# Kernel tuning notes

Measured on AMD Instinct MI355X. Metric: run time of the kernel, lower is better.

Reference implementation:

```python
import jax, jax.numpy as jnp
import numpy as np

B, S, H = 2, 2048, 2048
NH, NKV, HD = 16, 4, 128
GROUPS = NH // NKV  # 4
ROPE_BASE = 10000.0


def _rope_tables(seq_len, dim):
    inv_freq = 1.0 / (ROPE_BASE ** (jnp.arange(0, dim, 2, dtype=jnp.float32) / dim))
    t = jnp.arange(seq_len, dtype=jnp.float32)
    freqs = jnp.outer(t, inv_freq)            # [S, HD/2]
    emb = jnp.concatenate([freqs, freqs], -1)  # [S, HD]
    return jnp.cos(emb), jnp.sin(emb)


def _rotate_half(x):
    x1, x2 = x[..., : x.shape[-1] // 2], x[..., x.shape[-1] // 2:]
    return jnp.concatenate([-x2, x1], axis=-1)


def setup_inputs() -> dict:
    key = jax.random.key(0)
    ks = jax.random.split(key, 5)
    hidden_states = jax.random.normal(ks[0], (B, S, H), dtype=jnp.float32)
    wq = jax.random.normal(ks[1], (H, NH * HD), dtype=jnp.float32) * 0.02
    wk = jax.random.normal(ks[2], (H, NKV * HD), dtype=jnp.float32) * 0.02
    wv = jax.random.normal(ks[3], (H, NKV * HD), dtype=jnp.float32) * 0.02
    wo = jax.random.normal(ks[4], (NH * HD, H), dtype=jnp.float32) * 0.02
    # additive causal mask [1,1,S,S]
    causal = jnp.tril(jnp.ones((S, S), dtype=bool))
    attention_mask = jnp.where(causal, 0.0, jnp.finfo(jnp.float32).min)[None, None]
    return {"hidden_states": hidden_states, "attention_mask": attention_mask,
            "wq": wq, "wk": wk, "wv": wv, "wo": wo}


def reference(hidden_states, attention_mask, wq, wk, wv, wo):
    b, s, _ = hidden_states.shape
    # projections -> [B, heads, S, HD]
    q = (hidden_states @ wq).reshape(b, s, NH, HD).transpose(0, 2, 1, 3)
    k = (hidden_states @ wk).reshape(b, s, NKV, HD).transpose(0, 2, 1, 3)
    v = (hidden_states @ wv).reshape(b, s, NKV, HD).transpose(0, 2, 1, 3)
    cos, sin = _rope_tables(s, HD)             # [S, HD]
    cos = cos[None, None]; sin = sin[None, None]
    q = q * cos + _rotate_half(q) * sin
    k = k * cos + _rotate_half(k) * sin
    # GQA: repeat kv heads (matches repeat_interleave on dim=1)
    k = jnp.repeat(k, GROUPS, axis=1)
    v = jnp.repeat(v, GROUPS, axis=1)
    scores = jnp.einsum("bhqd,bhkd->bhqk", q, k) / jnp.sqrt(jnp.float32(HD))
    scores = scores + attention_mask
    probs = jax.nn.softmax(scores.astype(jnp.float32), axis=-1).astype(q.dtype)
    attn = jnp.einsum("bhqk,bhkd->bhqd", probs, v)
    attn = attn.transpose(0, 2, 1, 3).reshape(b, s, NH * HD)
    return attn @ wo
```

## Files before the change

### kernel.cpp

```cpp
#include <hip/hip_runtime.h>

typedef unsigned short u16;
typedef unsigned int u32;
typedef __attribute__((ext_vector_type(8))) __bf16 bf16x8;
typedef __attribute__((ext_vector_type(8))) u16 u16x8;
typedef __attribute__((ext_vector_type(4))) float f32x4;

#define B_ 2
#define S_ 2048
#define H_ 2048
#define NH_ 16
#define NKV_ 4
#define HD_ 128

__device__ __forceinline__ u16 f2bf(float f) {
  return __builtin_bit_cast(u16, static_cast<__bf16>(f));
}
__device__ __forceinline__ float bf2f(u16 v) {
  return __builtin_bit_cast(float, (u32)v << 16);
}
__device__ __forceinline__ void gl2lds16(const void* g, void* l) {
  __builtin_amdgcn_global_load_lds((const __attribute__((address_space(1))) u32*)g,
                                   (__attribute__((address_space(3))) u32*)l, 16, 0, 0);
}
__device__ __forceinline__ f32x4 mfma16(bf16x8 a, bf16x8 b, f32x4 c) {
  return __builtin_amdgcn_mfma_f32_16x16x32_bf16(a, b, c, 0, 0, 0);
}

__global__ __launch_bounds__(256) void cvt_f32_bf16(const float* __restrict__ in,
                                                    u16* __restrict__ out) {
  size_t i = ((size_t)blockIdx.x * 256 + threadIdx.x) * 8;
  const float4* p = (const float4*)(in + i);
  float4 a = p[0], b = p[1];
  u16x8 o;
  o[0] = f2bf(a.x); o[1] = f2bf(a.y); o[2] = f2bf(a.z); o[3] = f2bf(a.w);
  o[4] = f2bf(b.x); o[5] = f2bf(b.y); o[6] = f2bf(b.z); o[7] = f2bf(b.w);
  *(u16x8*)(out + i) = o;
}

__global__ __launch_bounds__(256) void transpose_qkv(const float* __restrict__ wq,
                                                     const float* __restrict__ wk,
                                                     const float* __restrict__ wv,
                                                     u16* __restrict__ out) {
  __shared__ float tl[32][33];
  int bx = blockIdx.x, by = blockIdx.y;
  int tx = threadIdx.x & 31, ty = threadIdx.x >> 5;
  int orow0 = bx * 32;
  const float* src;
  int scol0, C;
  if (orow0 < 2048)      { src = wq; scol0 = orow0;        C = 2048; }
  else if (orow0 < 2560) { src = wk; scol0 = orow0 - 2048; C = 512; }
  else                   { src = wv; scol0 = orow0 - 2560; C = 512; }
#pragma unroll
  for (int i = 0; i < 32; i += 8)
    tl[ty + i][tx] = src[(size_t)(by * 32 + ty + i) * C + scol0 + tx];
  __syncthreads();
#pragma unroll
  for (int i = 0; i < 32; i += 8)
    out[(size_t)(orow0 + ty + i) * 2048 + by * 32 + tx] = f2bf(tl[tx][ty + i]);
}

__global__ __launch_bounds__(256) void transpose_f32_bf16(const float* __restrict__ in,
                                                          u16* __restrict__ out,
                                                          int R, int C) {
  __shared__ float tl[32][33];
  int bx = blockIdx.x, by = blockIdx.y;
  int tx = threadIdx.x & 31, ty = threadIdx.x >> 5;
#pragma unroll
  for (int i = 0; i < 32; i += 8)
    tl[ty + i][tx] = in[(size_t)(by * 32 + ty + i) * C + bx * 32 + tx];
  __syncthreads();
#pragma unroll
  for (int i = 0; i < 32; i += 8)
    out[(size_t)(bx * 32 + ty + i) * R + by * 32 + tx] = f2bf(tl[tx][ty + i]);
}

__global__ __launch_bounds__(256) void transpose_v(const u16* __restrict__ kvb,
                                                   u16* __restrict__ vt) {
  __shared__ u16 tl[32][33];
  int sx = blockIdx.x, dx = blockIdx.y, b = blockIdx.z;
  int tx = threadIdx.x & 31, ty = threadIdx.x >> 5;
#pragma unroll
  for (int i = 0; i < 32; i += 8)
    tl[ty + i][tx] = kvb[(size_t)(b * S_ + sx * 32 + ty + i) * 1024 + 512 + dx * 32 + tx];
  __syncthreads();
#pragma unroll
  for (int i = 0; i < 32; i += 8)
    vt[(size_t)(b * 512 + dx * 32 + ty + i) * 2048 + sx * 32 + tx] = tl[tx][ty + i];
}

__global__ __launch_bounds__(256) void rope_kernel(u16* __restrict__ buf, int rstride,
                                                   int nhshift, float scale) {
  int idx = blockIdx.x * 256 + threadIdx.x;
  int grp = idx & 7;
  int h = (idx >> 3) & ((1 << nhshift) - 1);
  int tok = idx >> (3 + nhshift);
  int s = tok & (S_ - 1);
  u16* p = buf + (size_t)tok * rstride + (h << 7) + grp * 8;
  u16x8 lo = *(u16x8*)p;
  u16x8 hi = *(u16x8*)(p + 64);
  u16x8 olo, ohi;
#pragma unroll
  for (int j = 0; j < 8; j++) {
    int i = grp * 8 + j;
    float inv = exp2f((float)i * -0.20762050593045702f);
    float ang = (float)s * inv;
    float c = cosf(ang) * scale, sn = sinf(ang) * scale;
    float xl = bf2f(lo[j]), xh = bf2f(hi[j]);
    olo[j] = f2bf(xl * c - xh * sn);
    ohi[j] = f2bf(xh * c + xl * sn);
  }
  *(u16x8*)p = olo;
  *(u16x8*)(p + 64) = ohi;
}

template <int MODE>
__global__ __launch_bounds__(256) void gemm_bt(const u16* __restrict__ A,
                                               const u16* __restrict__ BT,
                                               void* __restrict__ C0,
                                               void* __restrict__ C1,
                                               int M, int N, int K) {
  __shared__ u16 As[2 * 128 * 32];
  __shared__ u16 Bs[2 * 128 * 32];
  const int Mt = M >> 7;
  const int nwg = gridDim.x;
  int wg = (blockIdx.x & 7) * (nwg >> 3) + (blockIdx.x >> 3);
  int tm = wg % Mt, tn = wg / Mt;
  const size_t m0 = (size_t)tm << 7, n0 = (size_t)tn << 7;
  const int tid = threadIdx.x;
  const int w = tid >> 6, lane = tid & 63;
  const int g = lane >> 4, l15 = lane & 15;
  const int wr = w >> 1, wc = w & 1;

  const int r0 = tid >> 2, s0 = tid & 3;
  const int r1 = (tid + 256) >> 2, s1 = (tid + 256) & 3;
  const u16* Ar0 = A + (m0 + r0) * K + s0 * 8;
  const u16* Ar1 = A + (m0 + r1) * K + s1 * 8;
  const u16* Br0 = BT + (n0 + r0) * K + s0 * 8;
  const u16* Br1 = BT + (n0 + r1) * K + s1 * 8;

  const f32x4 Z4 = {0.f, 0.f, 0.f, 0.f};
  f32x4 acc[4][4];
#pragma unroll
  for (int m = 0; m < 4; m++)
#pragma unroll
    for (int n = 0; n < 4; n++) acc[m][n] = Z4;

  gl2lds16(Ar0, &As[w * 512]);
  gl2lds16(Ar1, &As[w * 512 + 2048]);
  gl2lds16(Br0, &Bs[w * 512]);
  gl2lds16(Br1, &Bs[w * 512 + 2048]);

  const int nk = K >> 5;
  int cur = 0;
  for (int t = 0; t < nk; ++t) {
    if (t + 1 < nk) {
      const int k0 = (t + 1) << 5;
      const int nb = (cur ^ 1) << 12;
      gl2lds16(Ar0 + k0, &As[nb + w * 512]);
      gl2lds16(Ar1 + k0, &As[nb + w * 512 + 2048]);
      gl2lds16(Br0 + k0, &Bs[nb + w * 512]);
      gl2lds16(Br1 + k0, &Bs[nb + w * 512 + 2048]);
      asm volatile("s_waitcnt vmcnt(4)" ::: "memory");
    } else {
      asm volatile("s_waitcnt vmcnt(0)" ::: "memory");
    }
    __builtin_amdgcn_sched_barrier(0);
    __builtin_amdgcn_s_barrier();
    __builtin_amdgcn_sched_barrier(0);
    const int cb = cur << 12;
    bf16x8 af[4], bfr[4];
#pragma unroll
    for (int m = 0; m < 4; m++)
      af[m] = *(const bf16x8*)&As[cb + (wr * 64 + m * 16 + l15) * 32 + g * 8];
#pragma unroll
    for (int n = 0; n < 4; n++)
      bfr[n] = *(const bf16x8*)&Bs[cb + (wc * 64 + n * 16 + l15) * 32 + g * 8];
#pragma unroll
    for (int m = 0; m < 4; m++)
#pragma unroll
      for (int n = 0; n < 4; n++) acc[m][n] = mfma16(af[m], bfr[n], acc[m][n]);
    __builtin_amdgcn_sched_barrier(0);
    __builtin_amdgcn_s_barrier();
    __builtin_amdgcn_sched_barrier(0);
    cur ^= 1;
  }

  if (MODE == 2) {
    float* C = (float*)C0;
#pragma unroll
    for (int m = 0; m < 4; m++)
#pragma unroll
      for (int n = 0; n < 4; n++)
#pragma unroll
        for (int r = 0; r < 4; r++) {
          size_t row = m0 + wr * 64 + m * 16 + g * 4 + r;
          size_t col = n0 + wc * 64 + n * 16 + l15;
          C[row * (size_t)N + col] = acc[m][n][r];
        }
  } else {
    u16* C;
    size_t cs, cbase;
    if (n0 < 2048) { C = (u16*)C0; cs = 2048; cbase = n0; }
    else           { C = (u16*)C1; cs = 1024; cbase = n0 - 2048; }
#pragma unroll
    for (int m = 0; m < 4; m++)
#pragma unroll
      for (int n = 0; n < 4; n++)
#pragma unroll
        for (int r = 0; r < 4; r++) {
          size_t row = m0 + wr * 64 + m * 16 + g * 4 + r;
          C[row * cs + cbase + wc * 64 + n * 16 + l15] = f2bf(acc[m][n][r]);
        }
  }
}

__global__ __launch_bounds__(256) void attn_kernel(const u16* __restrict__ Qb,
                                                   const u16* __restrict__ KVb,
                                                   const u16* __restrict__ Vt,
                                                   u16* __restrict__ Ob) {
  __shared__ u16 Ks[2][64 * 128];
  __shared__ u16 Vs[2][128 * 64];
  __shared__ u16 Ps[4][16 * 72];
  const int pair = blockIdx.x, h = blockIdx.y, b = blockIdx.z;
  const int kvh = h >> 2;
  const int tid = threadIdx.x, w = tid >> 6, lane = tid & 63;
  const int g = lane >> 4, l15 = lane & 15;
  const f32x4 Z4 = {0.f, 0.f, 0.f, 0.f};
  u16x8 oneu;
#pragma unroll
  for (int j = 0; j < 8; j++) oneu[j] = 0x3f80;
  const bf16x8 ones = __builtin_bit_cast(bf16x8, oneu);

  const u16* Kbase = KVb + (size_t)b * S_ * 1024 + kvh * 128;
  const u16* Vbase = Vt + (size_t)(b * NKV_ + kvh) * HD_ * 2048;

  for (int half = 0; half < 2; ++half) {
    const int qt = half ? pair : 31 - pair;
    const int qrow0 = qt * 64 + w * 16;

    bf16x8 qf[4];
    const u16* qp = Qb + (size_t)(b * S_ + qrow0 + l15) * 2048 + h * 128;
#pragma unroll
    for (int ds = 0; ds < 4; ds++) qf[ds] = *(const bf16x8*)(qp + ds * 32 + g * 8);

    float m_r[4], l_r[4];
    f32x4 oa[8];
#pragma unroll
    for (int r = 0; r < 4; r++) { m_r[r] = -1e30f; l_r[r] = 0.f; }
#pragma unroll
    for (int n = 0; n < 8; n++) oa[n] = Z4;

    const int nt = qt + 1;
#pragma unroll
    for (int ro = 0; ro < 4; ++ro) {
      int c = ro * 256 + tid;
      int kv = c >> 4, p = c & 15;
      gl2lds16(Kbase + (size_t)kv * 1024 + 8 * (p ^ (kv & 15)), &Ks[0][ro * 2048 + w * 512]);
      int d = c >> 3, p2 = c & 7;
      gl2lds16(Vbase + (size_t)d * 2048 + 8 * (p2 ^ (d & 7)), &Vs[0][ro * 2048 + w * 512]);
    }
    __syncthreads();
    int cur = 0;

    for (int t = 0; t < nt; ++t) {
      const int kv0 = t * 64;
      if (t + 1 < nt) {
        const int nkv0 = kv0 + 64;
#pragma unroll
        for (int ro = 0; ro < 4; ++ro) {
          int c = ro * 256 + tid;
          int kv = c >> 4, p = c & 15;
          gl2lds16(Kbase + (size_t)(nkv0 + kv) * 1024 + 8 * (p ^ (kv & 15)),
                   &Ks[cur ^ 1][ro * 2048 + w * 512]);
          int d = c >> 3, p2 = c & 7;
          gl2lds16(Vbase + (size_t)d * 2048 + nkv0 + 8 * (p2 ^ (d & 7)),
                   &Vs[cur ^ 1][ro * 2048 + w * 512]);
        }
      }

      f32x4 sa[4];
#pragma unroll
      for (int c16 = 0; c16 < 4; c16++) sa[c16] = Z4;
      __builtin_amdgcn_s_setprio(1);
#pragma unroll
      for (int ds = 0; ds < 4; ++ds) {
#pragma unroll
        for (int c16 = 0; c16 < 4; ++c16) {
          bf16x8 kf = *(const bf16x8*)&Ks[cur][(c16 * 16 + l15) * 128 + ((ds * 4 + g) ^ l15) * 8];
          sa[c16] = mfma16(qf[ds], kf, sa[c16]);
        }
      }
      __builtin_amdgcn_s_setprio(0);

      if (kv0 + 63 > qrow0) {
#pragma unroll
        for (int c16 = 0; c16 < 4; c16++)
#pragma unroll
          for (int r = 0; r < 4; r++) {
            if (kv0 + c16 * 16 + l15 > qrow0 + g * 4 + r) sa[c16][r] = -1e30f;
          }
      }

      float lmax[4];
#pragma unroll
      for (int r = 0; r < 4; r++)
        lmax[r] = fmaxf(fmaxf(sa[0][r], sa[1][r]), fmaxf(sa[2][r], sa[3][r]));
      bool need = (lmax[0] > m_r[0] + 11.5415603f) || (lmax[1] > m_r[1] + 11.5415603f) ||
                  (lmax[2] > m_r[2] + 11.5415603f) || (lmax[3] > m_r[3] + 11.5415603f);
      if (__any(need)) {
        float pm[4];
#pragma unroll
        for (int r = 0; r < 4; r++) pm[r] = lmax[r];
#pragma unroll
        for (int off = 1; off < 16; off <<= 1)
#pragma unroll
          for (int r = 0; r < 4; r++) pm[r] = fmaxf(pm[r], __shfl_xor(pm[r], off));
#pragma unroll
        for (int r = 0; r < 4; r++) {
          float mn = fmaxf(m_r[r], pm[r]);
          float corr = exp2f(m_r[r] - mn);
          m_r[r] = mn;
          l_r[r] *= corr;
#pragma unroll
          for (int n = 0; n < 8; n++) oa[n][r] *= corr;
        }
      }

#pragma unroll
      for (int c16 = 0; c16 < 4; c16++)
#pragma unroll
        for (int r = 0; r < 4; r++)
          Ps[w][(g * 4 + r) * 72 + c16 * 16 + l15] =
              f2bf(exp2f(sa[c16][r] - m_r[r]));
      asm volatile("s_waitcnt lgkmcnt(0)" ::: "memory");
      __builtin_amdgcn_sched_barrier(0);

      f32x4 srow = Z4;
      __builtin_amdgcn_s_setprio(1);
#pragma unroll
      for (int ks = 0; ks < 2; ++ks) {
        bf16x8 pa = *(const bf16x8*)&Ps[w][l15 * 72 + ks * 32 + g * 8];
        srow = mfma16(pa, ones, srow);
#pragma unroll
        for (int n = 0; n < 8; n++) {
          bf16x8 vf = *(const bf16x8*)&Vs[cur][(n * 16 + l15) * 64 + (((ks * 4 + g) ^ (l15 & 7))) * 8];
          oa[n] = mfma16(pa, vf, oa[n]);
        }
      }
      __builtin_amdgcn_s_setprio(0);
#pragma unroll
      for (int r = 0; r < 4; r++) l_r[r] += srow[r];

      __syncthreads();
      cur ^= 1;
    }

    float inv[4];
#pragma unroll
    for (int r = 0; r < 4; r++) inv[r] = 1.0f / l_r[r];
#pragma unroll
    for (int n = 0; n < 8; n++)
#pragma unroll
      for (int r = 0; r < 4; r++) {
        size_t row = (size_t)b * S_ + qrow0 + g * 4 + r;
        Ob[row * 2048 + h * 128 + n * 16 + l15] = f2bf(oa[n][r] * inv[r]);
      }
  }
}

extern "C" void kernel_launch(void* const* d_in, const int* in_sizes, int n_in,
                              void* d_out, int out_size, void* d_ws, size_t ws_size,
                              hipStream_t stream) {
  const float* hid = (const float*)d_in[0];
  const float* wq = (const float*)d_in[2];
  const float* wk = (const float*)d_in[3];
  const float* wv = (const float*)d_in[4];
  const float* wo = (const float*)d_in[5];
  float* out = (float*)d_out;
  char* ws = (char*)d_ws;

  u16* hb     = (u16*)(ws);
  u16* wqkvT  = (u16*)(ws + (16u << 20));
  u16* Vt     = (u16*)(ws + (16u << 20));
  u16* woT    = (u16*)(ws + (20u << 20));
  u16* Qb     = (u16*)(ws + (28u << 20));
  u16* KVb    = (u16*)(ws + (44u << 20));

  cvt_f32_bf16<<<4096, 256, 0, stream>>>(hid, hb);
  transpose_qkv<<<dim3(96, 64), 256, 0, stream>>>(wq, wk, wv, wqkvT);

  gemm_bt<1><<<768, 256, 0, stream>>>(hb, wqkvT, Qb, KVb, 4096, 3072, 2048);

  rope_kernel<<<2048, 256, 0, stream>>>(Qb, 2048, 4, 0.1275179064f);
  rope_kernel<<<512, 256, 0, stream>>>(KVb, 1024, 2, 1.0f);

  transpose_v<<<dim3(64, 16, 2), 256, 0, stream>>>(KVb, Vt);
  transpose_f32_bf16<<<dim3(64, 64), 256, 0, stream>>>(wo, woT, 2048, 2048);

  attn_kernel<<<dim3(16, 16, 2), 256, 0, stream>>>(Qb, KVb, Vt, hb);

  gemm_bt<2><<<512, 256, 0, stream>>>(hb, woT, out, nullptr, 4096, 2048, 2048);
}
```

Before: 233.6 us.

## Fuse hidden-state bf16 conversion into QKV GEMM and tabulate RoPE cos/sin

```diff
diff --git a/kernel.cpp b/kernel.cpp
--- a/kernel.cpp
+++ b/kernel.cpp
@@ -25,17 +25,6 @@
 }
 __device__ __forceinline__ f32x4 mfma16(bf16x8 a, bf16x8 b, f32x4 c) {
   return __builtin_amdgcn_mfma_f32_16x16x32_bf16(a, b, c, 0, 0, 0);
-}
-
-__global__ __launch_bounds__(256) void cvt_f32_bf16(const float* __restrict__ in,
-                                                    u16* __restrict__ out) {
-  size_t i = ((size_t)blockIdx.x * 256 + threadIdx.x) * 8;
-  const float4* p = (const float4*)(in + i);
-  float4 a = p[0], b = p[1];
-  u16x8 o;
-  o[0] = f2bf(a.x); o[1] = f2bf(a.y); o[2] = f2bf(a.z); o[3] = f2bf(a.w);
-  o[4] = f2bf(b.x); o[5] = f2bf(b.y); o[6] = f2bf(b.z); o[7] = f2bf(b.w);
-  *(u16x8*)(out + i) = o;
 }
 
 __global__ __launch_bounds__(256) void transpose_qkv(const float* __restrict__ wq,
@@ -89,23 +78,32 @@
     vt[(size_t)(b * 512 + dx * 32 + ty + i) * 2048 + sx * 32 + tx] = tl[tx][ty + i];
 }
 
-__global__ __launch_bounds__(256) void rope_kernel(u16* __restrict__ buf, int rstride,
-                                                   int nhshift, float scale) {
+__global__ __launch_bounds__(256) void rope_table(float* __restrict__ tab) {
+  int idx = blockIdx.x * 256 + threadIdx.x;
+  int s = idx >> 6, i = idx & 63;
+  float inv = exp2f((float)i * -0.20762050593045702f);
+  float ang = (float)s * inv;
+  tab[2 * idx] = cosf(ang);
+  tab[2 * idx + 1] = sinf(ang);
+}
+
+__global__ __launch_bounds__(256) void rope_kernel(u16* __restrict__ buf,
+                                                   const float* __restrict__ tab,
+                                                   int rstride, int nhshift, float scale) {
   int idx = blockIdx.x * 256 + threadIdx.x;
   int grp = idx & 7;
   int h = (idx >> 3) & ((1 << nhshift) - 1);
   int tok = idx >> (3 + nhshift);
   int s = tok & (S_ - 1);
   u16* p = buf + (size_t)tok * rstride + (h << 7) + grp * 8;
+  const float2* tp = (const float2*)tab + (size_t)s * 64 + grp * 8;
   u16x8 lo = *(u16x8*)p;
   u16x8 hi = *(u16x8*)(p + 64);
   u16x8 olo, ohi;
 #pragma unroll
   for (int j = 0; j < 8; j++) {
-    int i = grp * 8 + j;
-    float inv = exp2f((float)i * -0.20762050593045702f);
-    float ang = (float)s * inv;
-    float c = cosf(ang) * scale, sn = sinf(ang) * scale;
+    float2 cs = tp[j];
+    float c = cs.x * scale, sn = cs.y * scale;
     float xl = bf2f(lo[j]), xh = bf2f(hi[j]);
     olo[j] = f2bf(xl * c - xh * sn);
     ohi[j] = f2bf(xh * c + xl * sn);
@@ -114,12 +112,125 @@
   *(u16x8*)(p + 64) = ohi;
 }
 
-template <int MODE>
-__global__ __launch_bounds__(256) void gemm_bt(const u16* __restrict__ A,
-                                               const u16* __restrict__ BT,
-                                               void* __restrict__ C0,
-                                               void* __restrict__ C1,
-                                               int M, int N, int K) {
+__global__ __launch_bounds__(256) void gemm_qkv(const float* __restrict__ A,
+                                                const u16* __restrict__ BT,
+                                                u16* __restrict__ Qb,
+                                                u16* __restrict__ KVb) {
+  const int K = 2048;
+  __shared__ u16 As[2 * 128 * 32];
+  __shared__ u16 Bs[2 * 128 * 32];
+  const int Mt = 32;
+  const int nwg = gridDim.x;
+  int wg = (blockIdx.x & 7) * (nwg >> 3) + (blockIdx.x >> 3);
+  int tm = wg % Mt, tn = wg / Mt;
+  const size_t m0 = (size_t)tm << 7, n0 = (size_t)tn << 7;
+  const int tid = threadIdx.x;
+  const int w = tid >> 6, lane = tid & 63;
+  const int g = lane >> 4, l15 = lane & 15;
+  const int wr = w >> 1, wc = w & 1;
+
+  const int r0 = tid >> 2, s0 = tid & 3;
+  const int r1 = (tid + 256) >> 2, s1 = (tid + 256) & 3;
+  const float* Af0 = A + (m0 + r0) * K + s0 * 8;
+  const float* Af1 = A + (m0 + r1) * K + s1 * 8;
+  const u16* Br0 = BT + (n0 + r0) * K + s0 * 8;
+  const u16* Br1 = BT + (n0 + r1) * K + s1 * 8;
+
+  const f32x4 Z4 = {0.f, 0.f, 0.f, 0.f};
+  f32x4 acc[4][4];
+#pragma unroll
+  for (int m = 0; m < 4; m++)
+#pragma unroll
+    for (int n = 0; n < 4; n++) acc[m][n] = Z4;
+
+  float4 pr0, pr1, pr2, pr3;
+  pr0 = *(const float4*)(Af0);      pr1 = *(const float4*)(Af0 + 4);
+  pr2 = *(const float4*)(Af1);      pr3 = *(const float4*)(Af1 + 4);
+  gl2lds16(Br0, &Bs[w * 512]);
+  gl2lds16(Br1, &Bs[w * 512 + 2048]);
+  {
+    u16x8 o;
+    o[0] = f2bf(pr0.x); o[1] = f2bf(pr0.y); o[2] = f2bf(pr0.z); o[3] = f2bf(pr0.w);
+    o[4] = f2bf(pr1.x); o[5] = f2bf(pr1.y); o[6] = f2bf(pr1.z); o[7] = f2bf(pr1.w);
+    *(u16x8*)&As[tid * 8] = o;
+    o[0] = f2bf(pr2.x); o[1] = f2bf(pr2.y); o[2] = f2bf(pr2.z); o[3] = f2bf(pr2.w);
+    o[4] = f2bf(pr3.x); o[5] = f2bf(pr3.y); o[6] = f2bf(pr3.z); o[7] = f2bf(pr3.w);
+    *(u16x8*)&As[2048 + tid * 8] = o;
+  }
+  pr0 = *(const float4*)(Af0 + 32); pr1 = *(const float4*)(Af0 + 36);
+  pr2 = *(const float4*)(Af1 + 32); pr3 = *(const float4*)(Af1 + 36);
+  asm volatile("s_waitcnt vmcnt(4)" ::: "memory");
+  asm volatile("s_waitcnt lgkmcnt(0)" ::: "memory");
+  __builtin_amdgcn_sched_barrier(0);
+  __builtin_amdgcn_s_barrier();
+  __builtin_amdgcn_sched_barrier(0);
+
+  const int nk = K >> 5;
+  int cur = 0;
+  for (int t = 0; t < nk; ++t) {
+    if (t + 1 < nk) {
+      const int k0 = (t + 1) << 5;
+      const int nb = (cur ^ 1) << 12;
+      gl2lds16(Br0 + k0, &Bs[nb + w * 512]);
+      gl2lds16(Br1 + k0, &Bs[nb + w * 512 + 2048]);
+      {
+        u16x8 o;
+        o[0] = f2bf(pr0.x); o[1] = f2bf(pr0.y); o[2] = f2bf(pr0.z); o[3] = f2bf(pr0.w);
+        o[4] = f2bf(pr1.x); o[5] = f2bf(pr1.y); o[6] = f2bf(pr1.z); o[7] = f2bf(pr1.w);
+        *(u16x8*)&As[nb + tid * 8] = o;
+        o[0] = f2bf(pr2.x); o[1] = f2bf(pr2.y); o[2] = f2bf(pr2.z); o[3] = f2bf(pr2.w);
+        o[4] = f2bf(pr3.x); o[5] = f2bf(pr3.y); o[6] = f2bf(pr3.z); o[7] = f2bf(pr3.w);
+        *(u16x8*)&As[nb + 2048 + tid * 8] = o;
+      }
+      if (t + 2 < nk) {
+        const int k2 = (t + 2) << 5;
+        pr0 = *(const float4*)(Af0 + k2);     pr1 = *(const float4*)(Af0 + k2 + 4);
+        pr2 = *(const float4*)(Af1 + k2);     pr3 = *(const float4*)(Af1 + k2 + 4);
+      }
+    } else {
+      asm volatile("s_waitcnt vmcnt(0)" ::: "memory");
+    }
+    asm volatile("s_waitcnt lgkmcnt(0)" ::: "memory");
+    __builtin_amdgcn_sched_barrier(0);
+    __builtin_amdgcn_s_barrier();
+    __builtin_amdgcn_sched_barrier(0);
+    const int cb = cur << 12;
+    bf16x8 af[4], bfr[4];
+#pragma unroll
+    for (int m = 0; m < 4; m++)
+      af[m] = *(const bf16x8*)&As[cb + (wr * 64 + m * 16 + l15) * 32 + g * 8];
+#pragma unroll
+    for (int n = 0; n < 4; n++)
+      bfr[n] = *(const bf16x8*)&Bs[cb + (wc * 64 + n * 16 + l15) * 32 + g * 8];
+#pragma unroll
+    for (int m = 0; m < 4; m++)
+#pragma unroll
+      for (int n = 0; n < 4; n++) acc[m][n] = mfma16(af[m], bfr[n], acc[m][n]);
+    __builtin_amdgcn_sched_barrier(0);
+    __builtin_amdgcn_s_barrier();
+    __builtin_amdgcn_sched_barrier(0);
+    cur ^= 1;
+  }
+
+  u16* C;
+  size_t cs, cbase;
+  if (n0 < 2048) { C = Qb; cs = 2048; cbase = n0; }
+  else           { C = KVb; cs = 1024; cbase = n0 - 2048; }
+#pragma unroll
+  for (int m = 0; m < 4; m++)
+#pragma unroll
+    for (int n = 0; n < 4; n++)
+#pragma unroll
+      for (int r = 0; r < 4; r++) {
+        size_t row = m0 + wr * 64 + m * 16 + g * 4 + r;
+        C[row * cs + cbase + wc * 64 + n * 16 + l15] = f2bf(acc[m][n][r]);
+      }
+}
+
+__global__ __launch_bounds__(256) void gemm_bt2(const u16* __restrict__ A,
+                                                const u16* __restrict__ BT,
+                                                float* __restrict__ C,
+                                                int M, int N, int K) {
   __shared__ u16 As[2 * 128 * 32];
   __shared__ u16 Bs[2 * 128 * 32];
   const int Mt = M >> 7;
@@ -186,33 +297,16 @@
     cur ^= 1;
   }
 
-  if (MODE == 2) {
-    float* C = (float*)C0;
-#pragma unroll
-    for (int m = 0; m < 4; m++)
-#pragma unroll
-      for (int n = 0; n < 4; n++)
-#pragma unroll
-        for (int r = 0; r < 4; r++) {
-          size_t row = m0 + wr * 64 + m * 16 + g * 4 + r;
-          size_t col = n0 + wc * 64 + n * 16 + l15;
-          C[row * (size_t)N + col] = acc[m][n][r];
-        }
-  } else {
-    u16* C;
-    size_t cs, cbase;
-    if (n0 < 2048) { C = (u16*)C0; cs = 2048; cbase = n0; }
-    else           { C = (u16*)C1; cs = 1024; cbase = n0 - 2048; }
-#pragma unroll
-    for (int m = 0; m < 4; m++)
-#pragma unroll
-      for (int n = 0; n < 4; n++)
-#pragma unroll
-        for (int r = 0; r < 4; r++) {
-          size_t row = m0 + wr * 64 + m * 16 + g * 4 + r;
-          C[row * cs + cbase + wc * 64 + n * 16 + l15] = f2bf(acc[m][n][r]);
-        }
-  }
+#pragma unroll
+  for (int m = 0; m < 4; m++)
+#pragma unroll
+    for (int n = 0; n < 4; n++)
+#pragma unroll
+      for (int r = 0; r < 4; r++) {
+        size_t row = m0 + wr * 64 + m * 16 + g * 4 + r;
+        size_t col = n0 + wc * 64 + n * 16 + l15;
+        C[row * (size_t)N + col] = acc[m][n][r];
+      }
 }
 
 __global__ __launch_bounds__(256) void attn_kernel(const u16* __restrict__ Qb,
@@ -383,22 +477,23 @@
   u16* hb     = (u16*)(ws);
   u16* wqkvT  = (u16*)(ws + (16u << 20));
   u16* Vt     = (u16*)(ws + (16u << 20));
+  float* tab  = (float*)(ws + (20u << 20));
   u16* woT    = (u16*)(ws + (20u << 20));
   u16* Qb     = (u16*)(ws + (28u << 20));
   u16* KVb    = (u16*)(ws + (44u << 20));
 
-  cvt_f32_bf16<<<4096, 256, 0, stream>>>(hid, hb);
   transpose_qkv<<<dim3(96, 64), 256, 0, stream>>>(wq, wk, wv, wqkvT);
 
-  gemm_bt<1><<<768, 256, 0, stream>>>(hb, wqkvT, Qb, KVb, 4096, 3072, 2048);
-
-  rope_kernel<<<2048, 256, 0, stream>>>(Qb, 2048, 4, 0.1275179064f);
-  rope_kernel<<<512, 256, 0, stream>>>(KVb, 1024, 2, 1.0f);
+  gemm_qkv<<<768, 256, 0, stream>>>(hid, wqkvT, Qb, KVb);
+
+  rope_table<<<512, 256, 0, stream>>>(tab);
+  rope_kernel<<<2048, 256, 0, stream>>>(Qb, tab, 2048, 4, 0.1275179064f);
+  rope_kernel<<<512, 256, 0, stream>>>(KVb, tab, 1024, 2, 1.0f);
 
   transpose_v<<<dim3(64, 16, 2), 256, 0, stream>>>(KVb, Vt);
   transpose_f32_bf16<<<dim3(64, 64), 256, 0, stream>>>(wo, woT, 2048, 2048);
 
   attn_kernel<<<dim3(16, 16, 2), 256, 0, stream>>>(Qb, KVb, Vt, hb);
 
-  gemm_bt<2><<<512, 256, 0, stream>>>(hb, woT, out, nullptr, 4096, 2048, 2048);
-}
+  gemm_bt2<<<512, 256, 0, stream>>>(hb, woT, out, 4096, 2048, 2048);
+}
```

New measurement: 240.3 us. +2.9%, slower.
